# Performance work log

Measured on AMD Instinct MI355X. Metric: run time of the kernel, lower is better.

## Reference

```python
import jax, jax.numpy as jnp
import numpy as np

MAX_DIS = 4  # max_displacement == pad_size


def setup_inputs() -> dict:
    key = jax.random.key(0)
    k1, k2 = jax.random.split(key)
    in1 = jax.random.normal(k1, (2, 64, 32, 32, 32), dtype=jnp.float32)
    in2 = jax.random.normal(k2, (2, 64, 32, 32, 32), dtype=jnp.float32)
    return {"in1": in1, "in2": in2}


def _corr3d(in1, in2, max_dis):
    # in1, in2: [B, C, H, W, D]
    B, C, H, W, D = in1.shape
    K = 2 * max_dis + 1
    pad = ((0, 0), (0, 0), (max_dis, max_dis), (max_dis, max_dis), (max_dis, max_dis))
    in2_pad = jnp.pad(in2, pad)  # [B, C, H+2m, W+2m, D+2m]
    # gather index for the depth axis: all K shifted windows at once
    idx_d = jnp.arange(K)[:, None] + jnp.arange(D)[None, :]  # [K, D]
    outs = []
    # loop over the (dy, dx) shift grid (fixed 9x9 structural loop);
    # the dz shifts and the channel reduction are fully vectorized.
    for dy in range(K):
        for dx in range(K):
            s = in2_pad[:, :, dy:dy + H, dx:dx + W, :]          # [B, C, H, W, D+2m]
            w = s[..., idx_d]                                   # [B, C, H, W, K, D]
            # sum over channels -> K correlation channels (dz inner)
            outs.append(jnp.einsum('bchwkd,bchwd->bkhwd', w, in1))
    # channel order matches torch: n = dy*K*K + dx*K + dz
    return jnp.concatenate(outs, axis=1)  # [B, K^3, H, W, D]


def reference(in1, in2):
    return _corr3d(in1, in2, MAX_DIS)
```

## Files before the change

kernel.cpp:

```cpp
#include <hip/hip_runtime.h>

typedef __fp16 h2 __attribute__((ext_vector_type(2)));
typedef __fp16 h8 __attribute__((ext_vector_type(8)));
typedef float f4 __attribute__((ext_vector_type(4)));

namespace {
constexpr int JSTR = 72;
constexpr int JN = 48;
constexpr int COLH = JN * JSTR;
}

__global__ __launch_bounds__(256, 8) void corr3d_mfma(
    const float* __restrict__ in1, const float* __restrict__ in2,
    float* __restrict__ out)
{
  __shared__ __align__(16) __fp16 colbuf[2][COLH];
  __shared__ __align__(16) float obuf[2][2 * 9 * 32];

  const int tid = threadIdx.x;
  const int blk = ((blockIdx.x & 7) << 8) | (blockIdx.x >> 3);
  const int half = blk & 1;
  const int w0 = ((blk >> 1) & 15) << 1;
  const int h = (blk >> 5) & 31;
  const int b = blk >> 10;
  const int ciLo = half ? 45 : 0;
  const int ciHi = half ? 90 : 45;

  const int lane = tid & 63;
  const int wv = tid >> 6;
  const int jb = (wv == 0) ? 0 : (wv == 3) ? 32 : 16;
  const int db = (wv >= 2) ? 16 : 0;
  const int l15 = lane & 15;
  const int lhi = lane >> 4;

  const float* in1b = in1 + ((size_t)b << 21);
  const float* in2b = in2 + ((size_t)b << 21);

  for (int i = tid; i < 1152; i += 256) {
    const int bu = i / 576;
    const int r = i - bu * 576;
    const int jrow = r / 36;
    const int cc = r - jrow * 36;
    const int j = (jrow < 4) ? jrow : jrow + 32;
    h2 z = {(__fp16)0.f, (__fp16)0.f};
    *(h2*)&colbuf[bu][j * JSTR + cc * 2] = z;
  }

  const int sd = tid & 31;
  const int scq = tid >> 5;

  auto stage = [&](const float* src, bool valid, __fp16* dst) {
#pragma unroll
    for (int it = 0; it < 4; ++it) {
      const int cp = scq + (it << 3);
      h2 v = {(__fp16)0.f, (__fp16)0.f};
      if (valid) {
        const float x = src[((size_t)(2 * cp) << 15) + sd];
        const float y = src[((size_t)(2 * cp + 1) << 15) + sd];
        v = __builtin_amdgcn_cvt_pkrtz(x, y);
      }
      *(h2*)&dst[(4 + sd) * JSTR + 2 * cp] = v;
    }
  };

  h8 bfr[2][2];
#pragma unroll
  for (int pos = 0; pos < 2; ++pos) {
    __syncthreads();
    stage(in1b + (h << 10) + ((w0 + pos) << 5), true, colbuf[0]);
    __syncthreads();
#pragma unroll
    for (int ch = 0; ch < 2; ++ch)
      bfr[pos][ch] =
          *(const h8*)&colbuf[0][(4 + db + l15) * JSTR + ch * 32 + (lhi << 3)];
  }
  __syncthreads();
  {
    const int hcn = ciLo / 10;
    const int wcn = ciLo - hcn * 10;
    const int hp = h - 4 + hcn, wp = w0 - 4 + wcn;
    const bool valid = ((unsigned)hp < 32u) && ((unsigned)wp < 32u);
    stage(in2b + (hp << 10) + (wp << 5), valid, colbuf[ciLo & 1]);
  }
  __syncthreads();

  int boff[4];
  unsigned bmask = 0;
#pragma unroll
  for (int r = 0; r < 4; ++r) {
    const int m = (lhi << 2) + r;
    const int dz = jb + m - db - l15;
    if ((unsigned)dz < 9u) bmask |= 1u << r;
    boff[r] = dz * 32 + db + l15;
  }

  for (int ci = ciLo; ci < ciHi; ++ci) {
    float lx[4], ly[4];
    bool nvalid = false;
    if (ci + 1 < ciHi) {
      const int cn = ci + 1;
      const int hcn = cn / 10;
      const int wcn = cn - hcn * 10;
      const int hp = h - 4 + hcn;
      const int wp = w0 - 4 + wcn;
      nvalid = ((unsigned)hp < 32u) && ((unsigned)wp < 32u);
      if (nvalid) {
        const float* src = in2b + (hp << 10) + (wp << 5);
#pragma unroll
        for (int it = 0; it < 4; ++it) {
          const int cp = scq + (it << 3);
          lx[it] = src[((size_t)(2 * cp) << 15) + sd];
          ly[it] = src[((size_t)(2 * cp + 1) << 15) + sd];
        }
      }
    }

    const int hc = ci / 10;
    const int wc = ci - hc * 10;
    const bool serve[2] = {wc <= 8, wc >= 1};

    const __fp16* cb = colbuf[ci & 1];
    float* ob = obuf[ci & 1];
    const h8 a0 = *(const h8*)&cb[(jb + l15) * JSTR + (lhi << 3)];
    const h8 a1 = *(const h8*)&cb[(jb + l15) * JSTR + 32 + (lhi << 3)];
#pragma unroll
    for (int pos = 0; pos < 2; ++pos) {
      if (serve[pos]) {
        f4 acc = {0.f, 0.f, 0.f, 0.f};
        acc = __builtin_amdgcn_mfma_f32_16x16x32_f16(a0, bfr[pos][0], acc, 0, 0, 0);
        acc = __builtin_amdgcn_mfma_f32_16x16x32_f16(a1, bfr[pos][1], acc, 0, 0, 0);
#pragma unroll
        for (int r = 0; r < 4; ++r)
          if (bmask & (1u << r)) ob[pos * 288 + boff[r]] = acc[r];
      }
    }

    if (ci > ciLo && tid < 144) {
      const int cprev = ci - 1;
      const int hcp = cprev / 10;
      const int wcp = cprev - hcp * 10;
      const int pos = tid >= 72;
      const int rr = tid - pos * 72;
      const int dz = rr >> 3;
      const int q = rr & 7;
      const bool sv = pos ? (wcp >= 1) : (wcp <= 8);
      if (sv) {
        const f4 v = *(const f4*)&obuf[cprev & 1][pos * 288 + dz * 32 + (q << 2)];
        const size_t ch = (size_t)(b * 729 + (hcp * 9 + (wcp - pos)) * 9 + dz);
        f4* dstp = (f4*)(out + (ch << 15) + (h << 10) + ((w0 + pos) << 5) + (q << 2));
        __builtin_nontemporal_store(v, dstp);
      }
    }

    if (ci + 1 < ciHi) {
#pragma unroll
      for (int it = 0; it < 4; ++it) {
        const int cp = scq + (it << 3);
        h2 v = {(__fp16)0.f, (__fp16)0.f};
        if (nvalid) v = __builtin_amdgcn_cvt_pkrtz(lx[it], ly[it]);
        *(h2*)&colbuf[(ci + 1) & 1][(4 + sd) * JSTR + 2 * cp] = v;
      }
    }

    __syncthreads();
  }

  {
    const int cl = ciHi - 1;
    const int hcp = cl / 10;
    const int wcp = cl - hcp * 10;
    if (tid < 144) {
      const int pos = tid >= 72;
      const int rr = tid - pos * 72;
      const int dz = rr >> 3;
      const int q = rr & 7;
      const bool sv = pos ? (wcp >= 1) : (wcp <= 8);
      if (sv) {
        const f4 v = *(const f4*)&obuf[cl & 1][pos * 288 + dz * 32 + (q << 2)];
        const size_t ch = (size_t)(b * 729 + (hcp * 9 + (wcp - pos)) * 9 + dz);
        f4* dstp = (f4*)(out + (ch << 15) + (h << 10) + ((w0 + pos) << 5) + (q << 2));
        __builtin_nontemporal_store(v, dstp);
      }
    }
  }
}

extern "C" void kernel_launch(void* const* d_in, const int* in_sizes, int n_in,
                              void* d_out, int out_size, void* d_ws, size_t ws_size,
                              hipStream_t stream) {
  const float* in1 = (const float*)d_in[0];
  const float* in2 = (const float*)d_in[1];
  float* out = (float*)d_out;
  corr3d_mfma<<<dim3(2048), dim3(256), 0, stream>>>(in1, in2, out);
}
```

Measured before the change: 253.3 us.

## Process four w positions per block to widen in2 column reuse

Each block now handles four consecutive w positions instead of two, iterating over a 9x12 grid of in2 columns split into four quarters of 27. Each staged in2 column is shared by up to four output positions via MFMA, which cuts in2 global loads and per-column overhead relative to the outputs produced. In exchange, each block holds more B-fragment registers, has a larger output buffer and a store loop that runs more than once per thread, and launch bounds drop to 7 blocks per SM. The colbuf row count is also trimmed to 40.

```diff
diff --git a/kernel.cpp b/kernel.cpp
--- a/kernel.cpp
+++ b/kernel.cpp
@@ -6,25 +6,25 @@
 
 namespace {
 constexpr int JSTR = 72;
-constexpr int JN = 48;
-constexpr int COLH = JN * JSTR;
+constexpr int JROWS = 40;
+constexpr int COLH = JROWS * JSTR;
 }
 
-__global__ __launch_bounds__(256, 8) void corr3d_mfma(
+__global__ __launch_bounds__(256, 7) void corr3d_mfma(
     const float* __restrict__ in1, const float* __restrict__ in2,
     float* __restrict__ out)
 {
   __shared__ __align__(16) __fp16 colbuf[2][COLH];
-  __shared__ __align__(16) float obuf[2][2 * 9 * 32];
+  __shared__ __align__(16) float obuf[2][4 * 288];
 
   const int tid = threadIdx.x;
   const int blk = ((blockIdx.x & 7) << 8) | (blockIdx.x >> 3);
-  const int half = blk & 1;
-  const int w0 = ((blk >> 1) & 15) << 1;
+  const int quarter = blk & 3;
+  const int w0 = ((blk >> 2) & 7) << 2;
   const int h = (blk >> 5) & 31;
   const int b = blk >> 10;
-  const int ciLo = half ? 45 : 0;
-  const int ciHi = half ? 90 : 45;
+  const int ciLo = quarter * 27;
+  const int ciHi = ciLo + 27;
 
   const int lane = tid & 63;
   const int wv = tid >> 6;
@@ -36,9 +36,9 @@
   const float* in1b = in1 + ((size_t)b << 21);
   const float* in2b = in2 + ((size_t)b << 21);
 
-  for (int i = tid; i < 1152; i += 256) {
-    const int bu = i / 576;
-    const int r = i - bu * 576;
+  for (int i = tid; i < 576; i += 256) {
+    const int bu = i / 288;
+    const int r = i - bu * 288;
     const int jrow = r / 36;
     const int cc = r - jrow * 36;
     const int j = (jrow < 4) ? jrow : jrow + 32;
@@ -63,9 +63,9 @@
     }
   };
 
-  h8 bfr[2][2];
+  h8 bfr[4][2];
 #pragma unroll
-  for (int pos = 0; pos < 2; ++pos) {
+  for (int pos = 0; pos < 4; ++pos) {
     __syncthreads();
     stage(in1b + (h << 10) + ((w0 + pos) << 5), true, colbuf[0]);
     __syncthreads();
@@ -76,31 +76,24 @@
   }
   __syncthreads();
   {
-    const int hcn = ciLo / 10;
-    const int wcn = ciLo - hcn * 10;
+    const int hcn = ciLo / 12;
+    const int wcn = ciLo - hcn * 12;
     const int hp = h - 4 + hcn, wp = w0 - 4 + wcn;
     const bool valid = ((unsigned)hp < 32u) && ((unsigned)wp < 32u);
     stage(in2b + (hp << 10) + (wp << 5), valid, colbuf[ciLo & 1]);
   }
   __syncthreads();
 
-  int boff[4];
-  unsigned bmask = 0;
-#pragma unroll
-  for (int r = 0; r < 4; ++r) {
-    const int m = (lhi << 2) + r;
-    const int dz = jb + m - db - l15;
-    if ((unsigned)dz < 9u) bmask |= 1u << r;
-    boff[r] = dz * 32 + db + l15;
-  }
+  const int mr = jb - db + (lhi << 2) - l15;
+  const int dzb = db + l15;
 
   for (int ci = ciLo; ci < ciHi; ++ci) {
     float lx[4], ly[4];
     bool nvalid = false;
     if (ci + 1 < ciHi) {
       const int cn = ci + 1;
-      const int hcn = cn / 10;
-      const int wcn = cn - hcn * 10;
+      const int hcn = cn / 12;
+      const int wcn = cn - hcn * 12;
       const int hp = h - 4 + hcn;
       const int wp = w0 - 4 + wcn;
       nvalid = ((unsigned)hp < 32u) && ((unsigned)wp < 32u);
@@ -115,40 +108,43 @@
       }
     }
 
-    const int hc = ci / 10;
-    const int wc = ci - hc * 10;
-    const bool serve[2] = {wc <= 8, wc >= 1};
+    const int hc = ci / 12;
+    const int wc = ci - hc * 12;
 
     const __fp16* cb = colbuf[ci & 1];
     float* ob = obuf[ci & 1];
     const h8 a0 = *(const h8*)&cb[(jb + l15) * JSTR + (lhi << 3)];
     const h8 a1 = *(const h8*)&cb[(jb + l15) * JSTR + 32 + (lhi << 3)];
 #pragma unroll
-    for (int pos = 0; pos < 2; ++pos) {
-      if (serve[pos]) {
+    for (int pos = 0; pos < 4; ++pos) {
+      if ((unsigned)(wc - pos) <= 8u) {
         f4 acc = {0.f, 0.f, 0.f, 0.f};
         acc = __builtin_amdgcn_mfma_f32_16x16x32_f16(a0, bfr[pos][0], acc, 0, 0, 0);
         acc = __builtin_amdgcn_mfma_f32_16x16x32_f16(a1, bfr[pos][1], acc, 0, 0, 0);
 #pragma unroll
-        for (int r = 0; r < 4; ++r)
-          if (bmask & (1u << r)) ob[pos * 288 + boff[r]] = acc[r];
+        for (int r = 0; r < 4; ++r) {
+          const int dz = mr + r;
+          if ((unsigned)dz < 9u) ob[pos * 288 + dz * 32 + dzb] = acc[r];
+        }
       }
     }
 
-    if (ci > ciLo && tid < 144) {
+    if (ci > ciLo) {
       const int cprev = ci - 1;
-      const int hcp = cprev / 10;
-      const int wcp = cprev - hcp * 10;
-      const int pos = tid >= 72;
-      const int rr = tid - pos * 72;
-      const int dz = rr >> 3;
-      const int q = rr & 7;
-      const bool sv = pos ? (wcp >= 1) : (wcp <= 8);
-      if (sv) {
-        const f4 v = *(const f4*)&obuf[cprev & 1][pos * 288 + dz * 32 + (q << 2)];
-        const size_t ch = (size_t)(b * 729 + (hcp * 9 + (wcp - pos)) * 9 + dz);
-        f4* dstp = (f4*)(out + (ch << 15) + (h << 10) + ((w0 + pos) << 5) + (q << 2));
-        __builtin_nontemporal_store(v, dstp);
+      const int hcp = cprev / 12;
+      const int wcp = cprev - hcp * 12;
+      const float* op = obuf[cprev & 1];
+      for (int s = tid; s < 288; s += 256) {
+        const int pos = s / 72;
+        const int rr = s - pos * 72;
+        const int dz = rr >> 3;
+        const int q = rr & 7;
+        if ((unsigned)(wcp - pos) <= 8u) {
+          const f4 v = *(const f4*)&op[pos * 288 + dz * 32 + (q << 2)];
+          const size_t chn = (size_t)(b * 729 + (hcp * 9 + (wcp - pos)) * 9 + dz);
+          f4* dstp = (f4*)(out + (chn << 15) + (h << 10) + ((w0 + pos) << 5) + (q << 2));
+          __builtin_nontemporal_store(v, dstp);
+        }
       }
     }
 
@@ -167,18 +163,18 @@
 
   {
     const int cl = ciHi - 1;
-    const int hcp = cl / 10;
-    const int wcp = cl - hcp * 10;
-    if (tid < 144) {
-      const int pos = tid >= 72;
-      const int rr = tid - pos * 72;
+    const int hcp = cl / 12;
+    const int wcp = cl - hcp * 12;
+    const float* op = obuf[cl & 1];
+    for (int s = tid; s < 288; s += 256) {
+      const int pos = s / 72;
+      const int rr = s - pos * 72;
       const int dz = rr >> 3;
       const int q = rr & 7;
-      const bool sv = pos ? (wcp >= 1) : (wcp <= 8);
-      if (sv) {
-        const f4 v = *(const f4*)&obuf[cl & 1][pos * 288 + dz * 32 + (q << 2)];
-        const size_t ch = (size_t)(b * 729 + (hcp * 9 + (wcp - pos)) * 9 + dz);
-        f4* dstp = (f4*)(out + (ch << 15) + (h << 10) + ((w0 + pos) << 5) + (q << 2));
+      if ((unsigned)(wcp - pos) <= 8u) {
+        const f4 v = *(const f4*)&op[pos * 288 + dz * 32 + (q << 2)];
+        const size_t chn = (size_t)(b * 729 + (hcp * 9 + (wcp - pos)) * 9 + dz);
+        f4* dstp = (f4*)(out + (chn << 15) + (h << 10) + ((w0 + pos) << 5) + (q << 2));
         __builtin_nontemporal_store(v, dstp);
       }
     }
```

Result: no change. 248.4 us (-1.9%).
